# Optimization experiments

Hardware: AMD Instinct MI355X
Metric: run time of the kernel (lower is better)

The kernel has to match this reference:

```python
import jax, jax.numpy as jnp
import numpy as np

N = 100000      # nodes
E = 1600000     # graph edges
P = 800000      # hypergraph incidence pairs
HE = 20000      # hyperedges
F_IN = 128      # node features
DIM = 64        # hidden dim (hard-coded in module)
NC = 40         # num_classes


def _lin_init(key, fan_in, fan_out):
    k1, k2 = jax.random.split(key)
    s = 1.0 / np.sqrt(fan_in)
    W = jax.random.uniform(k1, (fan_in, fan_out), jnp.float32, -s, s)
    b = jax.random.uniform(k2, (fan_out,), jnp.float32, -s, s)
    return W, b


def setup_inputs() -> dict:
    key = jax.random.key(0)
    ks = jax.random.split(key, 10)
    x = jax.random.normal(ks[0], (N, F_IN), jnp.float32)
    edge_index = jax.random.randint(ks[1], (2, E), 0, N, dtype=jnp.int64)
    node_idx = jax.random.randint(ks[2], (P,), 0, N, dtype=jnp.int64)
    he_idx = jax.random.randint(ks[3], (P,), 0, HE, dtype=jnp.int64)
    hyperedge_index = jnp.stack([node_idx, he_idx], axis=0)
    W_h1, b_h1 = _lin_init(ks[4], F_IN, DIM)
    W_h2, b_h2 = _lin_init(ks[5], DIM, DIM)
    W_c1, b_c1 = _lin_init(ks[6], F_IN + DIM, DIM)
    W_c2, b_c2 = _lin_init(ks[7], DIM, NC)
    W_lp, b_lp = _lin_init(ks[8], NC, NC)
    return dict(x=x, edge_index=edge_index, hyperedge_index=hyperedge_index,
                W_h1=W_h1, b_h1=b_h1, W_h2=W_h2, b_h2=b_h2,
                W_c1=W_c1, b_c1=b_c1, W_c2=W_c2, b_c2=b_c2,
                W_lp=W_lp, b_lp=b_lp)


def hypergraph_conv(x, node_idx, he_idx, W, b):
    # PyG HypergraphConv (no attention, hyperedge_weight = 1):
    # out = D^{-1} H B^{-1} H^T (x W) + b
    xw = x @ W                                    # [N, D]
    ones = jnp.ones(node_idx.shape[0], xw.dtype)
    Dn = jax.ops.segment_sum(ones, node_idx, num_segments=N)   # node degree
    Bh = jax.ops.segment_sum(ones, he_idx, num_segments=HE)    # hyperedge size
    D_inv = jnp.where(Dn > 0, 1.0 / Dn, 0.0)
    B_inv = jnp.where(Bh > 0, 1.0 / Bh, 0.0)
    # node -> hyperedge: m_e = (1/|e|) sum_{i in e} xw[i]
    msg1 = xw[node_idx] * B_inv[he_idx][:, None]               # [P, D]
    e_feat = jax.ops.segment_sum(msg1, he_idx, num_segments=HE)
    # hyperedge -> node: out_i = (1/deg(i)) sum_{e ni i} m_e
    msg2 = e_feat[he_idx] * D_inv[node_idx][:, None]           # [P, D]
    out = jax.ops.segment_sum(msg2, node_idx, num_segments=N)
    return out + b


def gcn_conv(x, edge_index, W, b):
    # PyG GCNConv: add self-loops, symmetric normalization
    xw = x @ W                                    # [N, D]
    loop = jnp.arange(N, dtype=edge_index.dtype)
    src = jnp.concatenate([edge_index[0], loop])
    dst = jnp.concatenate([edge_index[1], loop])
    deg = jax.ops.segment_sum(jnp.ones(dst.shape[0], xw.dtype), dst, num_segments=N)
    dis = jnp.where(deg > 0, jax.lax.rsqrt(deg), 0.0)
    norm = dis[src] * dis[dst]                    # [E+N]
    out = jax.ops.segment_sum(xw[src] * norm[:, None], dst, num_segments=N)
    return out + b


def reference(x, edge_index, hyperedge_index,
              W_h1, b_h1, W_h2, b_h2, W_c1, b_c1, W_c2, b_c2, W_lp, b_lp):
    node_idx, he_idx = hyperedge_index[0], hyperedge_index[1]
    x_hyper = jax.nn.relu(hypergraph_conv(x, node_idx, he_idx, W_h1, b_h1))
    # dropout is identity in eval mode
    x_hyper = hypergraph_conv(x_hyper, node_idx, he_idx, W_h2, b_h2)
    xc = jnp.concatenate([x, x_hyper], axis=1)    # [N, F_IN + DIM]
    x_gnn = jax.nn.relu(gcn_conv(xc, edge_index, W_c1, b_c1))
    x_gnn = gcn_conv(x_gnn, edge_index, W_c2, b_c2)
    return x_gnn @ W_lp + b_lp                     # [N, NC]
```

## Files before the change

kernel.cpp:

```cpp
#include <hip/hip_runtime.h>
#include <hip/hip_bf16.h>


typedef __attribute__((ext_vector_type(8))) short s16x8;
typedef __attribute__((ext_vector_type(4))) float f32x4;
typedef __attribute__((ext_vector_type(8))) float f32x8;

__device__ __forceinline__ float ldf(const void* p, int f32, long long i) {
    if (f32) return ((const float*)p)[i];
    unsigned v = ((unsigned)((const unsigned short*)p)[i]) << 16;
    return __uint_as_float(v);
}

__device__ __forceinline__ int ldi(const int* __restrict__ w, int i64, long long i, int lim) {
    int v = i64 ? w[2 * i] : w[i];
    return ((unsigned)v < (unsigned)lim) ? v : 0;
}

__device__ __forceinline__ float b2f(unsigned short u) {
    return __uint_as_float(((unsigned)u) << 16);
}
__device__ __forceinline__ unsigned short f2b(float f) {
    __hip_bfloat16 h = __float2bfloat16(f);
    return *reinterpret_cast<unsigned short*>(&h);
}
__device__ __forceinline__ f32x8 b2f8(s16x8 u) {
    f32x8 r;
#pragma unroll
    for (int q = 0; q < 8; q++) r[q] = b2f((unsigned short)u[q]);
    return r;
}
__device__ __forceinline__ s16x8 f2b8(f32x8 v) {
    s16x8 r;
#pragma unroll
    for (int q = 0; q < 8; q++) r[q] = (short)f2b(v[q]);
    return r;
}

__device__ int det_bf16_blk(const void* p, int nbytes, int* shcnt) {
    if (threadIdx.x == 0) *shcnt = 0;
    __syncthreads();
    const unsigned short* u = (const unsigned short*)p;
    int np = nbytes; if (np > 2048) np = 2048;
    int c = 0;
    for (int i = threadIdx.x; i < np; i += blockDim.x) {
        unsigned e = (u[i] >> 7) & 0xFFu;
        if (e != 0u && (e < 90u || e > 160u)) c++;
    }
    atomicAdd(shcnt, c);
    __syncthreads();
    int f = ((*shcnt) * 8 > np) ? 1 : 0;
    __syncthreads();
    return f;
}

__device__ int det_i64_blk(const int* w, int np, int* shcnt) {
    if (threadIdx.x == 0) *shcnt = 0;
    __syncthreads();
    int c = 0;
    for (int i = threadIdx.x; i < np; i += blockDim.x)
        if (w[2 * i + 1] != 0) c++;
    atomicAdd(shcnt, c);
    __syncthreads();
    int f = ((*shcnt) == 0) ? 1 : 0;
    __syncthreads();
    return f;
}

struct BP { const void* B; int nbytes; int K; int M; int Mp; unsigned short* out; };
struct D6 { const void* p[6]; int n[6]; int fi[6]; int i64[6]; };

__global__ void detprep_k(D6 d6, int* __restrict__ FL,
                          int* __restrict__ gBkt, int* __restrict__ done,
                          BP p0, BP p1, BP p2,
                          const void* Wc2, int szWc2, const void* Wlp, int szWlp,
                          const void* bc2, int szbc2, const void* blp, int szblp,
                          unsigned short* __restrict__ btl, float* __restrict__ bias2, int NC) {
    __shared__ int shcnt;
    int b = blockIdx.x, t = threadIdx.x;
    if (b == 0) {
        for (int i = t; i < 768; i += blockDim.x) gBkt[i] = 0;
        if (t == 0) done[0] = 0;
    }
    if (b < 6) {
        int f = d6.i64[b] ? det_i64_blk((const int*)d6.p[b], d6.n[b], &shcnt)
                          : det_bf16_blk(d6.p[b], d6.n[b], &shcnt);
        if (t == 0) FL[d6.fi[b]] = f;
        return;
    }
    if (b < 9) {
        BP p = (b == 6) ? p0 : (b == 7) ? p1 : p2;
        int fb = det_bf16_blk(p.B, p.nbytes, &shcnt);
        int tot = p.Mp * p.K;
        for (int e = t; e < tot; e += blockDim.x) {
            int m = e / p.K, k = e - m * p.K;
            float v = (m < p.M) ? ldf(p.B, fb, (long long)k * p.M + m) : 0.f;
            p.out[e] = f2b(v);
        }
        return;
    }
    int fw2 = det_bf16_blk(Wc2, szWc2, &shcnt);
    int flp = det_bf16_blk(Wlp, szWlp, &shcnt);
    int fb2 = det_bf16_blk(bc2, szbc2, &shcnt);
    int fbl = det_bf16_blk(blp, szblp, &shcnt);
    extern __shared__ float sm[];
    float* sW2 = sm;
    float* sLP = sm + 64 * NC;
    for (int e = t; e < 64 * NC; e += blockDim.x) sW2[e] = ldf(Wc2, fw2, e);
    for (int e = t; e < NC * NC; e += blockDim.x) sLP[e] = ldf(Wlp, flp, e);
    for (int e = t; e < 48 * 64; e += blockDim.x) btl[e] = 0;
    __syncthreads();
    for (int e = t; e < 64 * NC; e += blockDim.x) {
        int r = e / NC, c = e % NC;
        float s = 0.f;
        for (int k = 0; k < NC; k++) s = fmaf(sW2[r * NC + k], sLP[k * NC + c], s);
        btl[c * 64 + r] = f2b(s);
    }
    if (t < NC) {
        float s = ldf(blp, fbl, t);
        for (int k = 0; k < NC; k++) s = fmaf(ldf(bc2, fb2, k), sLP[k * NC + t], s);
        bias2[t] = s;
    }
}

struct Item { int b1; unsigned p1; int b2; unsigned p2; };

__device__ __forceinline__ Item decode(const int* __restrict__ ew, const int* __restrict__ hw,
                                       const int* __restrict__ FL, long long i,
                                       int E, int P, int N, int HE, int shN, int shH) {
    Item it; it.b2 = -1; it.p2 = 0;
    if (i < E) {
        int g = FL[11];
        int key = ldi(ew, g, (long long)E + i, N);
        int val = ldi(ew, g, i, N);
        it.b1 = key >> shN;
        it.p1 = ((unsigned)(key & ((1 << shN) - 1)) << 20) | (unsigned)val;
    } else {
        long long j = i - E;
        int g = FL[12];
        int nd = ldi(hw, g, j, N);
        int he = ldi(hw, g, (long long)P + j, HE);
        it.b1 = 256 + (nd >> shN);
        it.p1 = ((unsigned)(nd & ((1 << shN) - 1)) << 20) | (unsigned)he;
        it.b2 = 512 + (he >> shH);
        it.p2 = ((unsigned)(he & ((1 << shH) - 1)) << 20) | (unsigned)nd;
    }
    return it;
}

#define PCHUNK 8192
#define PTHREADS 1024

__global__ __launch_bounds__(PTHREADS)
void chunkhist_k(const int* __restrict__ ew, const int* __restrict__ hw,
                 const int* __restrict__ FL, int* __restrict__ gcnt,
                 int* __restrict__ chunkHist, int* __restrict__ done,
                 int* __restrict__ bkOff, int* __restrict__ gcur,
                 int E, int P, int N, int HE, int shN, int shH) {
    __shared__ int hist[768];
    int t = threadIdx.x;
    for (int b = t; b < 768; b += PTHREADS) hist[b] = 0;
    __syncthreads();
    long long T = (long long)E + P;
    long long start = (long long)blockIdx.x * PCHUNK;
    long long end = start + PCHUNK; if (end > T) end = T;
    for (long long i = start + t; i < end; i += PTHREADS) {
        Item it = decode(ew, hw, FL, i, E, P, N, HE, shN, shH);
        atomicAdd(&hist[it.b1], 1);
        if (it.b2 >= 0) atomicAdd(&hist[it.b2], 1);
    }
    __syncthreads();
    long long hbase = (long long)blockIdx.x * 768;
    for (int b = t; b < 768; b += PTHREADS) {
        int h = hist[b];
        chunkHist[hbase + b] = h;
        if (h) atomicAdd(&gcnt[b], h);
    }
    __syncthreads();
    __shared__ int isLast;
    if (t == 0) {
        __threadfence();
        isLast = (atomicAdd(done, 1) == (int)gridDim.x - 1);
    }
    __syncthreads();
    if (!isLast) return;
    __shared__ int sh[256];
    for (int c = 0; c < 3; c++) {
        int v = 0;
        if (t < 256) { v = atomicAdd(&gcnt[c * 256 + t], 0); sh[t] = v; }
        __syncthreads();
        for (int o = 1; o < 256; o <<= 1) {
            int y = (t < 256 && t >= o) ? sh[t - o] : 0;
            __syncthreads();
            if (t < 256) sh[t] += y;
            __syncthreads();
        }
        if (t < 256) {
            int excl = sh[t] - v;
            bkOff[c * 256 + t] = excl;
            long long rb = (c == 0) ? 0 : ((c == 1) ? (long long)E : (long long)E + P);
            gcur[c * 256 + t] = (int)(rb + excl);
        }
        __syncthreads();
    }
}

__global__ __launch_bounds__(PTHREADS)
void place_k(const int* __restrict__ ew, const int* __restrict__ hw,
             const int* __restrict__ FL, int* __restrict__ gcur,
             const int* __restrict__ chunkHist, unsigned* __restrict__ pbuf,
             int E, int P, int N, int HE, int shN, int shH) {
    __shared__ int cur[768];
    long long T = (long long)E + P;
    long long start = (long long)blockIdx.x * PCHUNK;
    long long end = start + PCHUNK; if (end > T) end = T;
    int t = threadIdx.x;
    long long hbase = (long long)blockIdx.x * 768;
    for (int b = t; b < 768; b += PTHREADS) {
        int h = chunkHist[hbase + b];
        cur[b] = h ? atomicAdd(&gcur[b], h) : 0;
    }
    __syncthreads();
    for (long long i = start + t; i < end; i += PTHREADS) {
        Item it = decode(ew, hw, FL, i, E, P, N, HE, shN, shH);
        int s1 = atomicAdd(&cur[it.b1], 1);
        pbuf[s1] = it.p1;
        if (it.b2 >= 0) {
            int s2 = atomicAdd(&cur[it.b2], 1);
            pbuf[s2] = it.p2;
        }
    }
}

__global__ void build_k(const unsigned* __restrict__ pbuf,
                        const int* __restrict__ gcnt, const int* __restrict__ bkOff,
                        int* __restrict__ eoff, int* __restrict__ ecnt, int* __restrict__ esrc,
                        int* __restrict__ poffN, int* __restrict__ pcntN, int* __restrict__ pheL,
                        int* __restrict__ poffH, int* __restrict__ pcntH, int* __restrict__ pniL,
                        float* __restrict__ dis, float* __restrict__ Dinv, float* __restrict__ Binv,
                        int E, int P, int N, int HE, int shN, int shH) {
    __shared__ int hist[512];
    __shared__ int offs[512];
    __shared__ int s2[256];
    int b = blockIdx.x, t = threadIdx.x;
    int csr = b >> 8, lb = b & 255;
    int sh    = (csr == 2) ? shH : shN;
    int nkeys = (csr == 2) ? HE : N;
    int span = 1 << sh;
    int keyBase = lb << sh;
    if (keyBase >= nkeys) return;
    int keyEnd = keyBase + span; if (keyEnd > nkeys) keyEnd = nkeys;
    int cnt = gcnt[b];
    long long rbase = (csr == 0) ? 0 : ((csr == 1) ? (long long)E : (long long)E + P);
    long long pstart = rbase + bkOff[b];
    int lstBase = bkOff[b];
    int* off  = (csr == 0) ? eoff : ((csr == 1) ? poffN : poffH);
    int* cntA = (csr == 0) ? ecnt : ((csr == 1) ? pcntN : pcntH);
    int* lst  = (csr == 0) ? esrc : ((csr == 1) ? pheL : pniL);

    for (int k = t; k < 512; k += 256) hist[k] = 0;
    __syncthreads();
    for (int i = t; i < cnt; i += 256)
        atomicAdd(&hist[pbuf[pstart + i] >> 20], 1);
    __syncthreads();
    int a0 = hist[2 * t], a1 = hist[2 * t + 1];
    s2[t] = a0 + a1;
    __syncthreads();
    for (int o = 1; o < 256; o <<= 1) {
        int y = (t >= o) ? s2[t - o] : 0;
        __syncthreads();
        s2[t] += y;
        __syncthreads();
    }
    int excl = s2[t] - (a0 + a1);
    offs[2 * t] = excl;
    offs[2 * t + 1] = excl + a0;
    __syncthreads();
    for (int k = keyBase + t; k < keyEnd; k += 256) {
        int h = hist[k - keyBase];
        off[k]  = lstBase + offs[k - keyBase];
        cntA[k] = h;
        if (csr == 0)      dis[k]  = rsqrtf((float)(h + 1));
        else if (csr == 1) Dinv[k] = h ? (1.f / (float)h) : 0.f;
        else               Binv[k] = h ? (1.f / (float)h) : 0.f;
    }
    __syncthreads();
    for (int i = t; i < cnt; i += 256) {
        unsigned u = pbuf[pstart + i];
        int lk = u >> 20;
        int slot = atomicAdd(&offs[lk], 1);
        lst[lstBase + slot] = (int)(u & 0xFFFFFu);
    }
}

__device__ __forceinline__ f32x8 gsum64(const unsigned short* __restrict__ src,
                                        const int* __restrict__ lst,
                                        int o, int c, int l, f32x8 a) {
    int j = 0;
    for (; j + 8 <= c; j += 8) {
        int s0 = lst[o + j], s1 = lst[o + j + 1], s2 = lst[o + j + 2], s3 = lst[o + j + 3];
        int s4 = lst[o + j + 4], s5 = lst[o + j + 5], s6 = lst[o + j + 6], s7 = lst[o + j + 7];
        f32x8 v0 = b2f8(*(const s16x8*)&src[((long long)s0 << 6) + l * 8]);
        f32x8 v1 = b2f8(*(const s16x8*)&src[((long long)s1 << 6) + l * 8]);
        f32x8 v2 = b2f8(*(const s16x8*)&src[((long long)s2 << 6) + l * 8]);
        f32x8 v3 = b2f8(*(const s16x8*)&src[((long long)s3 << 6) + l * 8]);
        f32x8 v4 = b2f8(*(const s16x8*)&src[((long long)s4 << 6) + l * 8]);
        f32x8 v5 = b2f8(*(const s16x8*)&src[((long long)s5 << 6) + l * 8]);
        f32x8 v6 = b2f8(*(const s16x8*)&src[((long long)s6 << 6) + l * 8]);
        f32x8 v7 = b2f8(*(const s16x8*)&src[((long long)s7 << 6) + l * 8]);
#pragma unroll
        for (int q = 0; q < 8; q++)
            a[q] += ((v0[q] + v1[q]) + (v2[q] + v3[q])) + ((v4[q] + v5[q]) + (v6[q] + v7[q]));
    }
    for (; j + 4 <= c; j += 4) {
        int s0 = lst[o + j], s1 = lst[o + j + 1], s2 = lst[o + j + 2], s3 = lst[o + j + 3];
        f32x8 v0 = b2f8(*(const s16x8*)&src[((long long)s0 << 6) + l * 8]);
        f32x8 v1 = b2f8(*(const s16x8*)&src[((long long)s1 << 6) + l * 8]);
        f32x8 v2 = b2f8(*(const s16x8*)&src[((long long)s2 << 6) + l * 8]);
        f32x8 v3 = b2f8(*(const s16x8*)&src[((long long)s3 << 6) + l * 8]);
#pragma unroll
        for (int q = 0; q < 8; q++) a[q] += (v0[q] + v1[q]) + (v2[q] + v3[q]);
    }
    for (; j < c; j++) {
        f32x8 v = b2f8(*(const s16x8*)&src[((long long)lst[o + j] << 6) + l * 8]);
#pragma unroll
        for (int q = 0; q < 8; q++) a[q] += v[q];
    }
    return a;
}

__global__ void gat_n2e_k(const unsigned short* __restrict__ xw, const int* __restrict__ off,
                          const int* __restrict__ cnt, const int* __restrict__ lst,
                          const float* __restrict__ Binv, unsigned short* __restrict__ ef, int HE) {
    int idx = blockIdx.x * blockDim.x + threadIdx.x;
    int e = idx >> 3, l = idx & 7;
    if (e >= HE) return;
    f32x8 a = {0.f, 0.f, 0.f, 0.f, 0.f, 0.f, 0.f, 0.f};
    a = gsum64(xw, lst, off[e], cnt[e], l, a);
    float bi = Binv[e];
#pragma unroll
    for (int q = 0; q < 8; q++) a[q] *= bi;
    *(s16x8*)&ef[((long long)e << 6) + l * 8] = f2b8(a);
}

template <bool RELU>
__global__ void gat_e2n_k(const unsigned short* __restrict__ ef, const int* __restrict__ off,
                          const int* __restrict__ cnt, const int* __restrict__ lst,
                          const float* __restrict__ Dinv, const void* __restrict__ bias,
                          const int* __restrict__ fb, unsigned short* __restrict__ out, int N) {
    int idx = blockIdx.x * blockDim.x + threadIdx.x;
    int w = idx >> 3, l = idx & 7;
    if (w >= N) return;
    f32x8 a = {0.f, 0.f, 0.f, 0.f, 0.f, 0.f, 0.f, 0.f};
    a = gsum64(ef, lst, off[w], cnt[w], l, a);
    float di = Dinv[w];
    int fbv = fb[0];
#pragma unroll
    for (int q = 0; q < 8; q++) {
        float bq = ldf(bias, fbv, l * 8 + q);
        a[q] = a[q] * di + bq;
        if (RELU) a[q] = fmaxf(a[q], 0.f);
    }
    *(s16x8*)&out[((long long)w << 6) + l * 8] = f2b8(a);
}

template <bool RELU>
__global__ void gcn_gat_k(const unsigned short* __restrict__ y, const int* __restrict__ off,
                          const int* __restrict__ cnt, const int* __restrict__ lst,
                          const float* __restrict__ dis, const void* __restrict__ bias,
                          const int* __restrict__ fb, unsigned short* __restrict__ out, int N) {
    int idx = blockIdx.x * blockDim.x + threadIdx.x;
    int w = idx >> 3, l = idx & 7;
    if (w >= N) return;
    f32x8 a = b2f8(*(const s16x8*)&y[((long long)w << 6) + l * 8]);
    a = gsum64(y, lst, off[w], cnt[w], l, a);
    float dd = dis[w];
    int fbv = fb[0];
#pragma unroll
    for (int q = 0; q < 8; q++) {
        float bq = ldf(bias, fbv, l * 8 + q);
        a[q] = a[q] * dd + bq;
        if (RELU) a[q] = fmaxf(a[q], 0.f);
    }
    *(s16x8*)&out[((long long)w << 6) + l * 8] = f2b8(a);
}

__global__ void gcn_gatM_k(const unsigned short* __restrict__ y2, const int* __restrict__ off,
                           const int* __restrict__ cnt, const int* __restrict__ lst,
                           const float* __restrict__ dis, const float* __restrict__ bias2,
                           float4* __restrict__ out4, int N, int NC) {
    int idx = blockIdx.x * blockDim.x + threadIdx.x;
    int wave = idx >> 6, l64 = idx & 63;
    int lpr = NC >> 3;
    int rpw = 64 / lpr;
    int grp = l64 / lpr, li = l64 - grp * lpr;
    int w = wave * rpw + grp;
    if (grp >= rpw || w >= N) return;
    int o = off[w], c = cnt[w];
    f32x8 a = b2f8(*(const s16x8*)&y2[(long long)w * NC + li * 8]);
    int j = 0;
    for (; j + 8 <= c; j += 8) {
        int s0 = lst[o + j], s1 = lst[o + j + 1], s2 = lst[o + j + 2], s3 = lst[o + j + 3];
        int s4 = lst[o + j + 4], s5 = lst[o + j + 5], s6 = lst[o + j + 6], s7 = lst[o + j + 7];
        f32x8 v0 = b2f8(*(const s16x8*)&y2[(long long)s0 * NC + li * 8]);
        f32x8 v1 = b2f8(*(const s16x8*)&y2[(long long)s1 * NC + li * 8]);
        f32x8 v2 = b2f8(*(const s16x8*)&y2[(long long)s2 * NC + li * 8]);
        f32x8 v3 = b2f8(*(const s16x8*)&y2[(long long)s3 * NC + li * 8]);
        f32x8 v4 = b2f8(*(const s16x8*)&y2[(long long)s4 * NC + li * 8]);
        f32x8 v5 = b2f8(*(const s16x8*)&y2[(long long)s5 * NC + li * 8]);
        f32x8 v6 = b2f8(*(const s16x8*)&y2[(long long)s6 * NC + li * 8]);
        f32x8 v7 = b2f8(*(const s16x8*)&y2[(long long)s7 * NC + li * 8]);
#pragma unroll
        for (int q = 0; q < 8; q++)
            a[q] += ((v0[q] + v1[q]) + (v2[q] + v3[q])) + ((v4[q] + v5[q]) + (v6[q] + v7[q]));
    }
    for (; j + 4 <= c; j += 4) {
        int s0 = lst[o + j], s1 = lst[o + j + 1], s2 = lst[o + j + 2], s3 = lst[o + j + 3];
        f32x8 v0 = b2f8(*(const s16x8*)&y2[(long long)s0 * NC + li * 8]);
        f32x8 v1 = b2f8(*(const s16x8*)&y2[(long long)s1 * NC + li * 8]);
        f32x8 v2 = b2f8(*(const s16x8*)&y2[(long long)s2 * NC + li * 8]);
        f32x8 v3 = b2f8(*(const s16x8*)&y2[(long long)s3 * NC + li * 8]);
#pragma unroll
        for (int q = 0; q < 8; q++) a[q] += (v0[q] + v1[q]) + (v2[q] + v3[q]);
    }
    for (; j < c; j++) {
        f32x8 v = b2f8(*(const s16x8*)&y2[(long long)lst[o + j] * NC + li * 8]);
#pragma unroll
        for (int q = 0; q < 8; q++) a[q] += v[q];
    }
    float dd = dis[w];
    const float4* b4 = (const float4*)&bias2[li * 8];
    float4 b0 = b4[0], b1 = b4[1];
    float4 lo = make_float4(a[0] * dd + b0.x, a[1] * dd + b0.y, a[2] * dd + b0.z, a[3] * dd + b0.w);
    float4 hi = make_float4(a[4] * dd + b1.x, a[5] * dd + b1.y, a[6] * dd + b1.z, a[7] * dd + b1.w);
    long long base = ((long long)w * NC + li * 8) >> 2;
    out4[base] = lo;
    out4[base + 1] = hi;
}

__device__ __forceinline__ s16x8 load8bf(const void* A, int af, long long base) {
    s16x8 o;
    if (af) {
        float4 v0 = *(const float4*)((const float*)A + base);
        float4 v1 = *(const float4*)((const float*)A + base + 4);
        o[0] = (short)f2b(v0.x); o[1] = (short)f2b(v0.y);
        o[2] = (short)f2b(v0.z); o[3] = (short)f2b(v0.w);
        o[4] = (short)f2b(v1.x); o[5] = (short)f2b(v1.y);
        o[6] = (short)f2b(v1.z); o[7] = (short)f2b(v1.w);
    } else {
        o = *(const s16x8*)&((const unsigned short*)A)[base];
    }
    return o;
}

template <int KK, int MM, bool CATMODE, bool ABF16, bool SCALE>
__global__ __launch_bounds__(256)
void gemm_mfma2_k(const void* __restrict__ A, const int* __restrict__ fA,
                  const unsigned short* __restrict__ A2,
                  const unsigned short* __restrict__ Bt,
                  const float* __restrict__ dscale,
                  unsigned short* __restrict__ C, int NR) {
    constexpr int MT = (MM + 15) / 16;
    static_assert(KK % 32 == 0, "K must be multiple of 32");

    const int t = threadIdx.x;
    const int wid = t >> 6, lane = t & 63;
    const long long r0 = ((long long)blockIdx.x * 4 + wid) * 32;
    if (r0 >= NR) return;

    const int af = fA ? fA[0] : 1;
    const int arow = lane & 15;
    const int kgrp = lane >> 4;
    long long ra = r0 + arow;      if (ra > NR - 1) ra = NR - 1;
    long long rb = r0 + 16 + arow; if (rb > NR - 1) rb = NR - 1;

    f32x4 acc0[MT] = {};
    f32x4 acc1[MT] = {};
#pragma unroll
    for (int kc = 0; kc < KK; kc += 32) {
        const int kb = kc + kgrp * 8;
        s16x8 a0, a1;
        if constexpr (CATMODE) {
            if (kc < 128) {
                a0 = load8bf(A, af, ra * 128 + kb);
                a1 = load8bf(A, af, rb * 128 + kb);
            } else {
                a0 = *(const s16x8*)&A2[ra * 64 + (kb - 128)];
                a1 = *(const s16x8*)&A2[rb * 64 + (kb - 128)];
            }
        } else if constexpr (ABF16) {
            a0 = *(const s16x8*)&((const unsigned short*)A)[ra * KK + kb];
            a1 = *(const s16x8*)&((const unsigned short*)A)[rb * KK + kb];
        } else {
            a0 = load8bf(A, af, ra * (long long)KK + kb);
            a1 = load8bf(A, af, rb * (long long)KK + kb);
        }
#pragma unroll
        for (int m = 0; m < MT; m++) {
            s16x8 b = *(const s16x8*)&Bt[(m * 16 + arow) * KK + kb];
            acc0[m] = __builtin_amdgcn_mfma_f32_16x16x32_bf16(a0, b, acc0[m], 0, 0, 0);
            acc1[m] = __builtin_amdgcn_mfma_f32_16x16x32_bf16(a1, b, acc1[m], 0, 0, 0);
        }
    }

    const int col0 = lane & 15;
    const int rsub = (lane >> 4) * 4;
#pragma unroll
    for (int h = 0; h < 2; h++) {
#pragma unroll
        for (int i = 0; i < 4; i++) {
            long long r = r0 + h * 16 + rsub + i;
            if (r < NR) {
                float s = SCALE ? dscale[r] : 1.f;
#pragma unroll
                for (int m = 0; m < MT; m++) {
                    int col = m * 16 + col0;
                    float val = h ? acc1[m][i] : acc0[m][i];
                    if (MT * 16 == MM || col < MM)
                        C[r * MM + col] = f2b(val * s);
                }
            }
        }
    }
}

static inline dim3 g1d(long long n, int b) { return dim3((unsigned)((n + b - 1) / b)); }
static inline int imin(int a, int b) { return a < b ? a : b; }

extern "C" void kernel_launch(void* const* d_in, const int* in_sizes, int n_in,
                              void* d_out, int out_size, void* d_ws, size_t ws_size,
                              hipStream_t stream) {
    const int N  = in_sizes[0] / 128;
    const int E  = in_sizes[1] / 2;
    const int P  = in_sizes[2] / 2;
    const int HE = 20000;
    const int NC = in_sizes[9] / 64;

    const void* x    = d_in[0];
    const int*  ew   = (const int*)d_in[1];
    const int*  hw   = (const int*)d_in[2];
    const void* W_h1 = d_in[3];
    const void* b_h1 = d_in[4];
    const void* W_h2 = d_in[5];
    const void* b_h2 = d_in[6];
    const void* W_c1 = d_in[7];
    const void* b_c1 = d_in[8];
    const void* W_c2 = d_in[9];
    const void* b_c2 = d_in[10];
    const void* W_lp = d_in[11];
    const void* b_lp = d_in[12];

    int shN = 0; while (((N - 1) >> shN) >= 256) shN++;
    int shH = 0; while (((HE - 1) >> shH) >= 256) shH++;

    long long T = (long long)E + P;
    int nChunks = (int)((T + PCHUNK - 1) / PCHUNK);

    char* wp = (char*)d_ws;
    auto allocF = [&](size_t n) { float* p = (float*)wp; wp += n * 4; return p; };
    auto allocI = [&](size_t n) { int* p = (int*)wp; wp += n * 4; return p; };
    unsigned short* ub  = (unsigned short*)allocF((size_t)N * 32);
    unsigned short* hb  = (unsigned short*)allocF((size_t)N * 32);
    unsigned short* efb = (unsigned short*)allocF((size_t)HE * 32);
    float* dis   = allocF(N);
    float* Dinv  = allocF(N);
    float* Binv  = allocF(HE);
    float* bias2 = allocF(NC);
    unsigned short* bt1 = (unsigned short*)allocF((size_t)64 * 128 / 2);
    unsigned short* bt2 = (unsigned short*)allocF((size_t)64 * 64 / 2);
    unsigned short* btc = (unsigned short*)allocF((size_t)64 * 192 / 2);
    unsigned short* btl = (unsigned short*)allocF((size_t)48 * 64 / 2);
    int* ecnt  = allocI(N);
    int* pcntN = allocI(N);
    int* pcntH = allocI(HE);
    int* eoff  = allocI(N);
    int* poffN = allocI(N);
    int* poffH = allocI(HE);
    int* esrc  = allocI(E);
    int* pheL  = allocI(P);
    int* pniL  = allocI(P);
    int* gBkt  = allocI(768);
    int* bkOff = allocI(768);
    int* gcur  = allocI(768);
    int* FL    = allocI(16);
    int* done  = allocI(4);
    int* chunkHist = allocI((size_t)nChunks * 768);
    unsigned* pbuf = (unsigned*)allocI((size_t)E + 2 * (size_t)P);

    dim3 b256(256), b1024(PTHREADS), d1(1);

    {
        D6 d6;
        d6.p[0] = x;    d6.n[0] = in_sizes[0];        d6.fi[0] = 0;  d6.i64[0] = 0;
        d6.p[1] = b_h1; d6.n[1] = in_sizes[4];        d6.fi[1] = 2;  d6.i64[1] = 0;
        d6.p[2] = b_h2; d6.n[2] = in_sizes[6];        d6.fi[2] = 4;  d6.i64[2] = 0;
        d6.p[3] = b_c1; d6.n[3] = in_sizes[8];        d6.fi[3] = 6;  d6.i64[3] = 0;
        d6.p[4] = ew;   d6.n[4] = imin(E, 1024);      d6.fi[4] = 11; d6.i64[4] = 1;
        d6.p[5] = hw;   d6.n[5] = imin(P, 1024);      d6.fi[5] = 12; d6.i64[5] = 1;
        BP p0 = {W_h1, in_sizes[3], 128, 64, 64, bt1};
        BP p1 = {W_h2, in_sizes[5],  64, 64, 64, bt2};
        BP p2 = {W_c1, in_sizes[7], 192, 64, 64, btc};
        detprep_k<<<dim3(10), b256, (64 * NC + NC * NC) * 4, stream>>>(
            d6, FL, gBkt, done, p0, p1, p2,
            W_c2, in_sizes[9], W_lp, in_sizes[11],
            b_c2, in_sizes[10], b_lp, in_sizes[12],
            btl, bias2, NC);
    }
    const int* fX   = FL + 0;
    const int* fbh1 = FL + 2;
    const int* fbh2 = FL + 4;
    const int* fbc1 = FL + 6;

    chunkhist_k<<<dim3(nChunks), b1024, 0, stream>>>(ew, hw, FL, gBkt, chunkHist, done,
                                                     bkOff, gcur, E, P, N, HE, shN, shH);
    place_k<<<dim3(nChunks), b1024, 0, stream>>>(ew, hw, FL, gcur, chunkHist, pbuf,
                                                 E, P, N, HE, shN, shH);
    build_k<<<dim3(768), b256, 0, stream>>>(pbuf, gBkt, bkOff,
                                            eoff, ecnt, esrc,
                                            poffN, pcntN, pheL,
                                            poffH, pcntH, pniL,
                                            dis, Dinv, Binv,
                                            E, P, N, HE, shN, shH);

    const dim3 mfmaGridN((N + 127) / 128);
    const dim3 mfmaGridH((HE + 127) / 128);
    const dim3 gatN8(g1d((long long)N * 8, 256));
    const dim3 gatH8(g1d((long long)HE * 8, 256));
    const int rpw = 64 / (NC >> 3);
    const dim3 gatNC(g1d((long long)((N + rpw - 1) / rpw) * 64, 256));

    gemm_mfma2_k<128, 64, false, false, false><<<mfmaGridN, b256, 0, stream>>>(
        x, fX, nullptr, bt1, nullptr, ub, N);
    gat_n2e_k<<<gatH8, b256, 0, stream>>>(ub, poffH, pcntH, pniL, Binv, efb, HE);
    gat_e2n_k<true><<<gatN8, b256, 0, stream>>>(efb, poffN, pcntN, pheL, Dinv, b_h1, fbh1, hb, N);

    gat_n2e_k<<<gatH8, b256, 0, stream>>>(hb, poffH, pcntH, pniL, Binv, efb, HE);
    gemm_mfma2_k<64, 64, false, true, false><<<mfmaGridH, b256, 0, stream>>>(
        efb, nullptr, nullptr, bt2, nullptr, ub, HE);
    gat_e2n_k<false><<<gatN8, b256, 0, stream>>>(ub, poffN, pcntN, pheL, Dinv, b_h2, fbh2, hb, N);

    gemm_mfma2_k<192, 64, true, false, true><<<mfmaGridN, b256, 0, stream>>>(
        x, fX, hb, btc, dis, ub, N);
    gcn_gat_k<true><<<gatN8, b256, 0, stream>>>(ub, eoff, ecnt, esrc, dis, b_c1, fbc1, hb, N);

    gemm_mfma2_k<64, 40, false, true, true><<<mfmaGridN, b256, 0, stream>>>(
        hb, nullptr, nullptr, btl, dis, ub, N);
    gcn_gatM_k<<<gatNC, b256, 0, stream>>>(ub, eoff, ecnt, esrc, dis, bias2, (float4*)d_out, N, NC);
}
```

Measured before the change: 410.5 us.

## Replace bucketed two-level CSR build with direct global-atomic count/scan/scatter

Replaces the three-pass bucket sort (per-chunk histograms, bucket placement into a packed buffer, per-bucket local sort) with a direct CSR build: global atomic degree counting, a two-level block scan for offsets, and a scatter using global atomic cursors. This removes the intermediate packed buffer and the chunk-histogram pass. In exchange it relies on many scattered global atomics over 100K-entry counters, and neighbor order within each segment becomes nondeterministic. A memset replaces the in-kernel counter reset.

Result: slower. 748.2 us (+82.3%).

```diff
diff --git a/kernel.cpp b/kernel.cpp
--- a/kernel.cpp
+++ b/kernel.cpp
@@ -71,17 +71,12 @@
 struct D6 { const void* p[6]; int n[6]; int fi[6]; int i64[6]; };
 
 __global__ void detprep_k(D6 d6, int* __restrict__ FL,
-                          int* __restrict__ gBkt, int* __restrict__ done,
                           BP p0, BP p1, BP p2,
                           const void* Wc2, int szWc2, const void* Wlp, int szWlp,
                           const void* bc2, int szbc2, const void* blp, int szblp,
                           unsigned short* __restrict__ btl, float* __restrict__ bias2, int NC) {
     __shared__ int shcnt;
     int b = blockIdx.x, t = threadIdx.x;
-    if (b == 0) {
-        for (int i = t; i < 768; i += blockDim.x) gBkt[i] = 0;
-        if (t == 0) done[0] = 0;
-    }
     if (b < 6) {
         int f = d6.i64[b] ? det_i64_blk((const int*)d6.p[b], d6.n[b], &shcnt)
                           : det_bf16_blk(d6.p[b], d6.n[b], &shcnt);
@@ -123,59 +118,54 @@
     }
 }
 
-struct Item { int b1; unsigned p1; int b2; unsigned p2; };
-
-__device__ __forceinline__ Item decode(const int* __restrict__ ew, const int* __restrict__ hw,
-                                       const int* __restrict__ FL, long long i,
-                                       int E, int P, int N, int HE, int shN, int shH) {
-    Item it; it.b2 = -1; it.p2 = 0;
+#define CTHREADS 1024
+
+__global__ __launch_bounds__(CTHREADS)
+void count_k(const int* __restrict__ ew, const int* __restrict__ hw,
+             const int* __restrict__ FL, int* __restrict__ cntAll,
+             int E, int P, int N, int HE) {
+    long long i = (long long)blockIdx.x * CTHREADS + threadIdx.x;
+    long long T = (long long)E + P;
+    if (i >= T) return;
     if (i < E) {
-        int g = FL[11];
-        int key = ldi(ew, g, (long long)E + i, N);
-        int val = ldi(ew, g, i, N);
-        it.b1 = key >> shN;
-        it.p1 = ((unsigned)(key & ((1 << shN) - 1)) << 20) | (unsigned)val;
+        int key = ldi(ew, FL[11], (long long)E + i, N);
+        atomicAdd(&cntAll[key], 1);
     } else {
         long long j = i - E;
         int g = FL[12];
         int nd = ldi(hw, g, j, N);
         int he = ldi(hw, g, (long long)P + j, HE);
-        it.b1 = 256 + (nd >> shN);
-        it.p1 = ((unsigned)(nd & ((1 << shN) - 1)) << 20) | (unsigned)he;
-        it.b2 = 512 + (he >> shH);
-        it.p2 = ((unsigned)(he & ((1 << shH) - 1)) << 20) | (unsigned)nd;
-    }
-    return it;
-}
-
-#define PCHUNK 8192
-#define PTHREADS 1024
-
-__global__ __launch_bounds__(PTHREADS)
-void chunkhist_k(const int* __restrict__ ew, const int* __restrict__ hw,
-                 const int* __restrict__ FL, int* __restrict__ gcnt,
-                 int* __restrict__ chunkHist, int* __restrict__ done,
-                 int* __restrict__ bkOff, int* __restrict__ gcur,
-                 int E, int P, int N, int HE, int shN, int shH) {
-    __shared__ int hist[768];
-    int t = threadIdx.x;
-    for (int b = t; b < 768; b += PTHREADS) hist[b] = 0;
-    __syncthreads();
-    long long T = (long long)E + P;
-    long long start = (long long)blockIdx.x * PCHUNK;
-    long long end = start + PCHUNK; if (end > T) end = T;
-    for (long long i = start + t; i < end; i += PTHREADS) {
-        Item it = decode(ew, hw, FL, i, E, P, N, HE, shN, shH);
-        atomicAdd(&hist[it.b1], 1);
-        if (it.b2 >= 0) atomicAdd(&hist[it.b2], 1);
-    }
-    __syncthreads();
-    long long hbase = (long long)blockIdx.x * 768;
-    for (int b = t; b < 768; b += PTHREADS) {
-        int h = hist[b];
-        chunkHist[hbase + b] = h;
-        if (h) atomicAdd(&gcnt[b], h);
-    }
+        atomicAdd(&cntAll[N + nd], 1);
+        atomicAdd(&cntAll[2 * N + he], 1);
+    }
+}
+
+__global__ __launch_bounds__(CTHREADS)
+void scan_k(const int* __restrict__ cntAll,
+            int* __restrict__ eoff, int* __restrict__ poffN, int* __restrict__ poffH,
+            int* __restrict__ bsum, int* __restrict__ gpref, int* __restrict__ done,
+            int N, int HE) {
+    __shared__ int sh[CTHREADS];
+    int b = blockIdx.x, t = threadIdx.x;
+    int nb0 = (N + CTHREADS - 1) / CTHREADS;
+    int nb2 = (HE + CTHREADS - 1) / CTHREADS;
+    int seg, lb, L, cntBase; int* offA;
+    if (b < nb0)            { seg = 0; lb = b;            L = N;  cntBase = 0;     offA = eoff;  }
+    else if (b < 2 * nb0)   { seg = 1; lb = b - nb0;      L = N;  cntBase = N;     offA = poffN; }
+    else                    { seg = 2; lb = b - 2 * nb0;  L = HE; cntBase = 2 * N; offA = poffH; }
+    int k = lb * CTHREADS + t;
+    int valid = (k < L);
+    int c = valid ? cntAll[cntBase + k] : 0;
+    sh[t] = c;
+    __syncthreads();
+    for (int o = 1; o < CTHREADS; o <<= 1) {
+        int y = (t >= o) ? sh[t - o] : 0;
+        __syncthreads();
+        sh[t] += y;
+        __syncthreads();
+    }
+    if (valid) offA[k] = sh[t] - c;
+    if (t == CTHREADS - 1) bsum[b] = sh[t];
     __syncthreads();
     __shared__ int isLast;
     if (t == 0) {
@@ -184,112 +174,72 @@
     }
     __syncthreads();
     if (!isLast) return;
-    __shared__ int sh[256];
-    for (int c = 0; c < 3; c++) {
+    __shared__ int sb[256];
+    int segStart[4] = {0, nb0, 2 * nb0, 2 * nb0 + nb2};
+    for (int s = 0; s < 3; s++) {
+        int s0 = segStart[s], nbS = segStart[s + 1] - s0;
         int v = 0;
-        if (t < 256) { v = atomicAdd(&gcnt[c * 256 + t], 0); sh[t] = v; }
+        if (t < nbS) { v = atomicAdd(&bsum[s0 + t], 0); sb[t] = v; }
         __syncthreads();
         for (int o = 1; o < 256; o <<= 1) {
-            int y = (t < 256 && t >= o) ? sh[t - o] : 0;
+            int y = (t < nbS && t >= o) ? sb[t - o] : 0;
             __syncthreads();
-            if (t < 256) sh[t] += y;
+            if (t < nbS) sb[t] += y;
             __syncthreads();
         }
-        if (t < 256) {
-            int excl = sh[t] - v;
-            bkOff[c * 256 + t] = excl;
-            long long rb = (c == 0) ? 0 : ((c == 1) ? (long long)E : (long long)E + P);
-            gcur[c * 256 + t] = (int)(rb + excl);
-        }
+        if (t < nbS) gpref[s0 + t] = sb[t] - v;
         __syncthreads();
     }
 }
 
-__global__ __launch_bounds__(PTHREADS)
-void place_k(const int* __restrict__ ew, const int* __restrict__ hw,
-             const int* __restrict__ FL, int* __restrict__ gcur,
-             const int* __restrict__ chunkHist, unsigned* __restrict__ pbuf,
-             int E, int P, int N, int HE, int shN, int shH) {
-    __shared__ int cur[768];
+__global__ __launch_bounds__(CTHREADS)
+void addback_k(const int* __restrict__ cntAll, const int* __restrict__ gpref,
+               int* __restrict__ eoff, int* __restrict__ poffN, int* __restrict__ poffH,
+               int* __restrict__ curE, int* __restrict__ curN, int* __restrict__ curH,
+               float* __restrict__ dis, float* __restrict__ Dinv, float* __restrict__ Binv,
+               int N, int HE) {
+    int b = blockIdx.x, t = threadIdx.x;
+    int nb0 = (N + CTHREADS - 1) / CTHREADS;
+    int seg, lb, L, cntBase; int* offA; int* curA;
+    if (b < nb0)            { seg = 0; lb = b;            L = N;  cntBase = 0;     offA = eoff;  curA = curE; }
+    else if (b < 2 * nb0)   { seg = 1; lb = b - nb0;      L = N;  cntBase = N;     offA = poffN; curA = curN; }
+    else                    { seg = 2; lb = b - 2 * nb0;  L = HE; cntBase = 2 * N; offA = poffH; curA = curH; }
+    int k = lb * CTHREADS + t;
+    if (k >= L) return;
+    int g = gpref[b];
+    int o = offA[k] + g;
+    offA[k] = o;
+    curA[k] = o;
+    int c = cntAll[cntBase + k];
+    if (seg == 0)      dis[k]  = rsqrtf((float)(c + 1));
+    else if (seg == 1) Dinv[k] = c ? (1.f / (float)c) : 0.f;
+    else               Binv[k] = c ? (1.f / (float)c) : 0.f;
+}
+
+__global__ __launch_bounds__(CTHREADS)
+void scatter_k(const int* __restrict__ ew, const int* __restrict__ hw,
+               const int* __restrict__ FL,
+               int* __restrict__ curE, int* __restrict__ curN, int* __restrict__ curH,
+               int* __restrict__ esrc, int* __restrict__ pheL, int* __restrict__ pniL,
+               int E, int P, int N, int HE) {
+    long long i = (long long)blockIdx.x * CTHREADS + threadIdx.x;
     long long T = (long long)E + P;
-    long long start = (long long)blockIdx.x * PCHUNK;
-    long long end = start + PCHUNK; if (end > T) end = T;
-    int t = threadIdx.x;
-    long long hbase = (long long)blockIdx.x * 768;
-    for (int b = t; b < 768; b += PTHREADS) {
-        int h = chunkHist[hbase + b];
-        cur[b] = h ? atomicAdd(&gcur[b], h) : 0;
-    }
-    __syncthreads();
-    for (long long i = start + t; i < end; i += PTHREADS) {
-        Item it = decode(ew, hw, FL, i, E, P, N, HE, shN, shH);
-        int s1 = atomicAdd(&cur[it.b1], 1);
-        pbuf[s1] = it.p1;
-        if (it.b2 >= 0) {
-            int s2 = atomicAdd(&cur[it.b2], 1);
-            pbuf[s2] = it.p2;
-        }
-    }
-}
-
-__global__ void build_k(const unsigned* __restrict__ pbuf,
-                        const int* __restrict__ gcnt, const int* __restrict__ bkOff,
-                        int* __restrict__ eoff, int* __restrict__ ecnt, int* __restrict__ esrc,
-                        int* __restrict__ poffN, int* __restrict__ pcntN, int* __restrict__ pheL,
-                        int* __restrict__ poffH, int* __restrict__ pcntH, int* __restrict__ pniL,
-                        float* __restrict__ dis, float* __restrict__ Dinv, float* __restrict__ Binv,
-                        int E, int P, int N, int HE, int shN, int shH) {
-    __shared__ int hist[512];
-    __shared__ int offs[512];
-    __shared__ int s2[256];
-    int b = blockIdx.x, t = threadIdx.x;
-    int csr = b >> 8, lb = b & 255;
-    int sh    = (csr == 2) ? shH : shN;
-    int nkeys = (csr == 2) ? HE : N;
-    int span = 1 << sh;
-    int keyBase = lb << sh;
-    if (keyBase >= nkeys) return;
-    int keyEnd = keyBase + span; if (keyEnd > nkeys) keyEnd = nkeys;
-    int cnt = gcnt[b];
-    long long rbase = (csr == 0) ? 0 : ((csr == 1) ? (long long)E : (long long)E + P);
-    long long pstart = rbase + bkOff[b];
-    int lstBase = bkOff[b];
-    int* off  = (csr == 0) ? eoff : ((csr == 1) ? poffN : poffH);
-    int* cntA = (csr == 0) ? ecnt : ((csr == 1) ? pcntN : pcntH);
-    int* lst  = (csr == 0) ? esrc : ((csr == 1) ? pheL : pniL);
-
-    for (int k = t; k < 512; k += 256) hist[k] = 0;
-    __syncthreads();
-    for (int i = t; i < cnt; i += 256)
-        atomicAdd(&hist[pbuf[pstart + i] >> 20], 1);
-    __syncthreads();
-    int a0 = hist[2 * t], a1 = hist[2 * t + 1];
-    s2[t] = a0 + a1;
-    __syncthreads();
-    for (int o = 1; o < 256; o <<= 1) {
-        int y = (t >= o) ? s2[t - o] : 0;
-        __syncthreads();
-        s2[t] += y;
-        __syncthreads();
-    }
-    int excl = s2[t] - (a0 + a1);
-    offs[2 * t] = excl;
-    offs[2 * t + 1] = excl + a0;
-    __syncthreads();
-    for (int k = keyBase + t; k < keyEnd; k += 256) {
-        int h = hist[k - keyBase];
-        off[k]  = lstBase + offs[k - keyBase];
-        cntA[k] = h;
-        if (csr == 0)      dis[k]  = rsqrtf((float)(h + 1));
-        else if (csr == 1) Dinv[k] = h ? (1.f / (float)h) : 0.f;
-        else               Binv[k] = h ? (1.f / (float)h) : 0.f;
-    }
-    __syncthreads();
-    for (int i = t; i < cnt; i += 256) {
-        unsigned u = pbuf[pstart + i];
-        int lk = u >> 20;
-        int slot = atomicAdd(&offs[lk], 1);
-        lst[lstBase + slot] = (int)(u & 0xFFFFFu);
+    if (i >= T) return;
+    if (i < E) {
+        int g = FL[11];
+        int key = ldi(ew, g, (long long)E + i, N);
+        int val = ldi(ew, g, i, N);
+        int pos = atomicAdd(&curE[key], 1);
+        esrc[pos] = val;
+    } else {
+        long long j = i - E;
+        int g = FL[12];
+        int nd = ldi(hw, g, j, N);
+        int he = ldi(hw, g, (long long)P + j, HE);
+        int p1 = atomicAdd(&curN[nd], 1);
+        pheL[p1] = he;
+        int p2 = atomicAdd(&curH[he], 1);
+        pniL[p2] = nd;
     }
 }
 
@@ -550,11 +500,11 @@
     const void* W_lp = d_in[11];
     const void* b_lp = d_in[12];
 
-    int shN = 0; while (((N - 1) >> shN) >= 256) shN++;
-    int shH = 0; while (((HE - 1) >> shH) >= 256) shH++;
-
     long long T = (long long)E + P;
-    int nChunks = (int)((T + PCHUNK - 1) / PCHUNK);
+    int nbT = (int)((T + CTHREADS - 1) / CTHREADS);
+    int nb0 = (N + CTHREADS - 1) / CTHREADS;
+    int nb2 = (HE + CTHREADS - 1) / CTHREADS;
+    int NB  = 2 * nb0 + nb2;
 
     char* wp = (char*)d_ws;
     auto allocF = [&](size_t n) { float* p = (float*)wp; wp += n * 4; return p; };
@@ -570,24 +520,25 @@
     unsigned short* bt2 = (unsigned short*)allocF((size_t)64 * 64 / 2);
     unsigned short* btc = (unsigned short*)allocF((size_t)64 * 192 / 2);
     unsigned short* btl = (unsigned short*)allocF((size_t)48 * 64 / 2);
-    int* ecnt  = allocI(N);
-    int* pcntN = allocI(N);
-    int* pcntH = allocI(HE);
-    int* eoff  = allocI(N);
-    int* poffN = allocI(N);
-    int* poffH = allocI(HE);
-    int* esrc  = allocI(E);
-    int* pheL  = allocI(P);
-    int* pniL  = allocI(P);
-    int* gBkt  = allocI(768);
-    int* bkOff = allocI(768);
-    int* gcur  = allocI(768);
-    int* FL    = allocI(16);
-    int* done  = allocI(4);
-    int* chunkHist = allocI((size_t)nChunks * 768);
-    unsigned* pbuf = (unsigned*)allocI((size_t)E + 2 * (size_t)P);
-
-    dim3 b256(256), b1024(PTHREADS), d1(1);
+    int* cntAll = allocI((size_t)2 * N + HE + 4);
+    int* done   = cntAll + 2 * N + HE;
+    int* eoff   = allocI(N);
+    int* poffN  = allocI(N);
+    int* poffH  = allocI(HE);
+    int* curE   = allocI(N);
+    int* curN   = allocI(N);
+    int* curH   = allocI(HE);
+    int* esrc   = allocI(E);
+    int* pheL   = allocI(P);
+    int* pniL   = allocI(P);
+    int* bsum   = allocI(256);
+    int* gpref  = allocI(256);
+    int* FL     = allocI(16);
+    const int* ecnt  = cntAll;
+    const int* pcntN = cntAll + N;
+    const int* pcntH = cntAll + 2 * N;
+
+    dim3 b256(256), b1024(CTHREADS), d1(1);
 
     {
         D6 d6;
@@ -601,7 +552,7 @@
         BP p1 = {W_h2, in_sizes[5],  64, 64, 64, bt2};
         BP p2 = {W_c1, in_sizes[7], 192, 64, 64, btc};
         detprep_k<<<dim3(10), b256, (64 * NC + NC * NC) * 4, stream>>>(
-            d6, FL, gBkt, done, p0, p1, p2,
+            d6, FL, p0, p1, p2,
             W_c2, in_sizes[9], W_lp, in_sizes[11],
             b_c2, in_sizes[10], b_lp, in_sizes[12],
             btl, bias2, NC);
@@ -611,16 +562,14 @@
     const int* fbh2 = FL + 4;
     const int* fbc1 = FL + 6;
 
-    chunkhist_k<<<dim3(nChunks), b1024, 0, stream>>>(ew, hw, FL, gBkt, chunkHist, done,
-                                                     bkOff, gcur, E, P, N, HE, shN, shH);
-    place_k<<<dim3(nChunks), b1024, 0, stream>>>(ew, hw, FL, gcur, chunkHist, pbuf,
-                                                 E, P, N, HE, shN, shH);
-    build_k<<<dim3(768), b256, 0, stream>>>(pbuf, gBkt, bkOff,
-                                            eoff, ecnt, esrc,
-                                            poffN, pcntN, pheL,
-                                            poffH, pcntH, pniL,
-                                            dis, Dinv, Binv,
-                                            E, P, N, HE, shN, shH);
+    hipMemsetAsync(cntAll, 0, ((size_t)2 * N + HE + 4) * 4, stream);
+    count_k<<<dim3(nbT), b1024, 0, stream>>>(ew, hw, FL, cntAll, E, P, N, HE);
+    scan_k<<<dim3(NB), b1024, 0, stream>>>(cntAll, eoff, poffN, poffH,
+                                           bsum, gpref, done, N, HE);
+    addback_k<<<dim3(NB), b1024, 0, stream>>>(cntAll, gpref, eoff, poffN, poffH,
+                                              curE, curN, curH, dis, Dinv, Binv, N, HE);
+    scatter_k<<<dim3(nbT), b1024, 0, stream>>>(ew, hw, FL, curE, curN, curH,
+                                               esrc, pheL, pniL, E, P, N, HE);
 
     const dim3 mfmaGridN((N + 127) / 128);
     const dim3 mfmaGridH((HE + 127) / 128);
```

## Fuse CSR build and first X·W_h1 GEMM into one heterogeneous launch

Applied to the files above, without the earlier changes.

The CSR build kernel and the first node-feature GEMM (x @ W_h1) are independent, so they are merged into one kernel whose first 768 blocks do the build and the remaining blocks do the GEMM. This removes one launch and lets the GEMM overlap the irregular, atomic-heavy build. The histogram pass also gets a slimmer decode that computes only bucket ids and skips the payload packing. In exchange, the kernel's resources are set by whichever body is heavier, and the GEMM now goes through a separate hand-written path instead of the templated one.

Result: no change. 416.0 us (+1.4%).

```diff
diff --git a/kernel.cpp b/kernel.cpp
--- a/kernel.cpp
+++ b/kernel.cpp
@@ -148,6 +148,23 @@
     return it;
 }
 
+__device__ __forceinline__ void decode_hist(const int* __restrict__ ew, const int* __restrict__ hw,
+                                            const int* __restrict__ FL, long long i,
+                                            int E, int P, int N, int HE, int shN, int shH,
+                                            int& b1, int& b2) {
+    if (i < E) {
+        int key = ldi(ew, FL[11], (long long)E + i, N);
+        b1 = key >> shN; b2 = -1;
+    } else {
+        long long j = i - E;
+        int g = FL[12];
+        int nd = ldi(hw, g, j, N);
+        int he = ldi(hw, g, (long long)P + j, HE);
+        b1 = 256 + (nd >> shN);
+        b2 = 512 + (he >> shH);
+    }
+}
+
 #define PCHUNK 8192
 #define PTHREADS 1024
 
@@ -165,9 +182,10 @@
     long long start = (long long)blockIdx.x * PCHUNK;
     long long end = start + PCHUNK; if (end > T) end = T;
     for (long long i = start + t; i < end; i += PTHREADS) {
-        Item it = decode(ew, hw, FL, i, E, P, N, HE, shN, shH);
-        atomicAdd(&hist[it.b1], 1);
-        if (it.b2 >= 0) atomicAdd(&hist[it.b2], 1);
+        int b1, b2;
+        decode_hist(ew, hw, FL, i, E, P, N, HE, shN, shH, b1, b2);
+        atomicAdd(&hist[b1], 1);
+        if (b2 >= 0) atomicAdd(&hist[b2], 1);
     }
     __syncthreads();
     long long hbase = (long long)blockIdx.x * 768;
@@ -232,17 +250,33 @@
     }
 }
 
-__global__ void build_k(const unsigned* __restrict__ pbuf,
-                        const int* __restrict__ gcnt, const int* __restrict__ bkOff,
-                        int* __restrict__ eoff, int* __restrict__ ecnt, int* __restrict__ esrc,
-                        int* __restrict__ poffN, int* __restrict__ pcntN, int* __restrict__ pheL,
-                        int* __restrict__ poffH, int* __restrict__ pcntH, int* __restrict__ pniL,
-                        float* __restrict__ dis, float* __restrict__ Dinv, float* __restrict__ Binv,
-                        int E, int P, int N, int HE, int shN, int shH) {
+__device__ __forceinline__ s16x8 load8bf(const void* A, int af, long long base) {
+    s16x8 o;
+    if (af) {
+        float4 v0 = *(const float4*)((const float*)A + base);
+        float4 v1 = *(const float4*)((const float*)A + base + 4);
+        o[0] = (short)f2b(v0.x); o[1] = (short)f2b(v0.y);
+        o[2] = (short)f2b(v0.z); o[3] = (short)f2b(v0.w);
+        o[4] = (short)f2b(v1.x); o[5] = (short)f2b(v1.y);
+        o[6] = (short)f2b(v1.z); o[7] = (short)f2b(v1.w);
+    } else {
+        o = *(const s16x8*)&((const unsigned short*)A)[base];
+    }
+    return o;
+}
+
+__device__ void build_body(int b,
+                           const unsigned* __restrict__ pbuf,
+                           const int* __restrict__ gcnt, const int* __restrict__ bkOff,
+                           int* __restrict__ eoff, int* __restrict__ ecnt, int* __restrict__ esrc,
+                           int* __restrict__ poffN, int* __restrict__ pcntN, int* __restrict__ pheL,
+                           int* __restrict__ poffH, int* __restrict__ pcntH, int* __restrict__ pniL,
+                           float* __restrict__ dis, float* __restrict__ Dinv, float* __restrict__ Binv,
+                           int E, int P, int N, int HE, int shN, int shH) {
     __shared__ int hist[512];
     __shared__ int offs[512];
     __shared__ int s2[256];
-    int b = blockIdx.x, t = threadIdx.x;
+    int t = threadIdx.x;
     int csr = b >> 8, lb = b & 255;
     int sh    = (csr == 2) ? shH : shN;
     int nkeys = (csr == 2) ? HE : N;
@@ -290,6 +324,69 @@
         int lk = u >> 20;
         int slot = atomicAdd(&offs[lk], 1);
         lst[lstBase + slot] = (int)(u & 0xFFFFFu);
+    }
+}
+
+__device__ void gemm128_body(const void* __restrict__ A, const int* __restrict__ fA,
+                             const unsigned short* __restrict__ Bt,
+                             unsigned short* __restrict__ C, int NR, int bid) {
+    const int t = threadIdx.x;
+    const int wid = t >> 6, lane = t & 63;
+    const long long r0 = ((long long)bid * 4 + wid) * 32;
+    if (r0 >= NR) return;
+    const int af = fA[0];
+    const int arow = lane & 15;
+    const int kgrp = lane >> 4;
+    long long ra = r0 + arow;      if (ra > NR - 1) ra = NR - 1;
+    long long rb = r0 + 16 + arow; if (rb > NR - 1) rb = NR - 1;
+    f32x4 acc0[4] = {};
+    f32x4 acc1[4] = {};
+#pragma unroll
+    for (int kc = 0; kc < 128; kc += 32) {
+        const int kb = kc + kgrp * 8;
+        s16x8 a0 = load8bf(A, af, ra * 128 + kb);
+        s16x8 a1 = load8bf(A, af, rb * 128 + kb);
+#pragma unroll
+        for (int m = 0; m < 4; m++) {
+            s16x8 b = *(const s16x8*)&Bt[(m * 16 + arow) * 128 + kb];
+            acc0[m] = __builtin_amdgcn_mfma_f32_16x16x32_bf16(a0, b, acc0[m], 0, 0, 0);
+            acc1[m] = __builtin_amdgcn_mfma_f32_16x16x32_bf16(a1, b, acc1[m], 0, 0, 0);
+        }
+    }
+    const int col0 = lane & 15;
+    const int rsub = (lane >> 4) * 4;
+#pragma unroll
+    for (int h = 0; h < 2; h++) {
+#pragma unroll
+        for (int i = 0; i < 4; i++) {
+            long long r = r0 + h * 16 + rsub + i;
+            if (r < NR) {
+#pragma unroll
+                for (int m = 0; m < 4; m++) {
+                    float val = h ? acc1[m][i] : acc0[m][i];
+                    C[r * 64 + m * 16 + col0] = f2b(val);
+                }
+            }
+        }
+    }
+}
+
+__global__ __launch_bounds__(256)
+void buildgemm_k(const unsigned* __restrict__ pbuf,
+                 const int* __restrict__ gcnt, const int* __restrict__ bkOff,
+                 int* __restrict__ eoff, int* __restrict__ ecnt, int* __restrict__ esrc,
+                 int* __restrict__ poffN, int* __restrict__ pcntN, int* __restrict__ pheL,
+                 int* __restrict__ poffH, int* __restrict__ pcntH, int* __restrict__ pniL,
+                 float* __restrict__ dis, float* __restrict__ Dinv, float* __restrict__ Binv,
+                 const void* __restrict__ x, const int* __restrict__ fX,
+                 const unsigned short* __restrict__ bt1, unsigned short* __restrict__ ub,
+                 int E, int P, int N, int HE, int shN, int shH) {
+    if (blockIdx.x < 768) {
+        build_body(blockIdx.x, pbuf, gcnt, bkOff, eoff, ecnt, esrc,
+                   poffN, pcntN, pheL, poffH, pcntH, pniL,
+                   dis, Dinv, Binv, E, P, N, HE, shN, shH);
+    } else {
+        gemm128_body(x, fX, bt1, ub, N, blockIdx.x - 768);
     }
 }
 
@@ -436,21 +533,6 @@
     long long base = ((long long)w * NC + li * 8) >> 2;
     out4[base] = lo;
     out4[base + 1] = hi;
-}
-
-__device__ __forceinline__ s16x8 load8bf(const void* A, int af, long long base) {
-    s16x8 o;
-    if (af) {
-        float4 v0 = *(const float4*)((const float*)A + base);
-        float4 v1 = *(const float4*)((const float*)A + base + 4);
-        o[0] = (short)f2b(v0.x); o[1] = (short)f2b(v0.y);
-        o[2] = (short)f2b(v0.z); o[3] = (short)f2b(v0.w);
-        o[4] = (short)f2b(v1.x); o[5] = (short)f2b(v1.y);
-        o[6] = (short)f2b(v1.z); o[7] = (short)f2b(v1.w);
-    } else {
-        o = *(const s16x8*)&((const unsigned short*)A)[base];
-    }
-    return o;
 }
 
 template <int KK, int MM, bool CATMODE, bool ABF16, bool SCALE>
@@ -615,12 +697,15 @@
                                                      bkOff, gcur, E, P, N, HE, shN, shH);
     place_k<<<dim3(nChunks), b1024, 0, stream>>>(ew, hw, FL, gcur, chunkHist, pbuf,
                                                  E, P, N, HE, shN, shH);
-    build_k<<<dim3(768), b256, 0, stream>>>(pbuf, gBkt, bkOff,
-                                            eoff, ecnt, esrc,
-                                            poffN, pcntN, pheL,
-                                            poffH, pcntH, pniL,
-                                            dis, Dinv, Binv,
-                                            E, P, N, HE, shN, shH);
+    {
+        int gemmBlocks = (N + 127) / 128;
+        buildgemm_k<<<dim3(768 + gemmBlocks), b256, 0, stream>>>(
+            pbuf, gBkt, bkOff,
+            eoff, ecnt, esrc, poffN, pcntN, pheL, poffH, pcntH, pniL,
+            dis, Dinv, Binv,
+            x, fX, bt1, ub,
+            E, P, N, HE, shN, shH);
+    }
 
     const dim3 mfmaGridN((N + 127) / 128);
     const dim3 mfmaGridH((HE + 127) / 128);
@@ -629,8 +714,6 @@
     const int rpw = 64 / (NC >> 3);
     const dim3 gatNC(g1d((long long)((N + rpw - 1) / rpw) * 64, 256));
 
-    gemm_mfma2_k<128, 64, false, false, false><<<mfmaGridN, b256, 0, stream>>>(
-        x, fX, nullptr, bt1, nullptr, ub, N);
     gat_n2e_k<<<gatH8, b256, 0, stream>>>(ub, poffH, pcntH, pniL, Binv, efb, HE);
     gat_e2n_k<true><<<gatN8, b256, 0, stream>>>(efb, poffN, pcntN, pheL, Dinv, b_h1, fbh1, hb, N);
 
```
